# Kernel optimization log

Measured on AMD Instinct MI355X. Metric: run time of the kernel, lower is better.

## Reference

```python
import jax, jax.numpy as jnp
import numpy as np

# video grid and attention geometry (must match init_kwargs)
F_T, H_T, W_T = 4, 32, 32
K = 3                      # kernel_size (odd)
P = K // 2
T = F_T * H_T * W_T        # max_num_tokens = 4096
HEADS = 8
DIM_HEAD = 64
SCALE = DIM_HEAD ** -0.5
DIM = 512
INNER = HEADS * DIM_HEAD


def _build_window_indices():
    # flat token index grid, padded with sentinel T (out-of-range -> zero row after gather)
    idx = np.arange(T).reshape(F_T, H_T, W_T)
    padded = np.full((F_T + 2 * P, H_T + 2 * P, W_T + 2 * P), T, dtype=np.int64)
    padded[P:P + F_T, P:P + H_T, P:P + W_T] = idx
    # [T, K^3] neighborhood indices, kernel offsets in (kf, kh, kw) C-order (matches unfoldNd)
    win = np.lib.stride_tricks.sliding_window_view(padded, (K, K, K)).reshape(T, K ** 3)
    # causal: mask keys whose flat index is strictly in the future of the query
    causal = np.arange(T)[:, None] < win
    causal = np.concatenate([np.zeros((T, 1), dtype=bool), causal], axis=1)  # BOS column never masked
    return jnp.asarray(win), jnp.asarray(causal)

WIN_IDX, CAUSAL_MASK = _build_window_indices()


def setup_inputs() -> dict:
    key = jax.random.key(0)
    k0, k1, k2, k3 = jax.random.split(key, 4)
    n = T  # 1 BOS + (T-1) video tokens; padding logic pads body to exactly T tokens
    x = jax.random.normal(k0, (2, n, DIM), dtype=jnp.float32)
    Wq = jax.random.normal(k1, (DIM, INNER), dtype=jnp.float32) * (DIM ** -0.5)
    Wkv = jax.random.normal(k2, (DIM, 2 * INNER), dtype=jnp.float32) * (DIM ** -0.5)
    Wo = jax.random.normal(k3, (INNER, DIM), dtype=jnp.float32) * (INNER ** -0.5)
    bo = jnp.zeros((DIM,), dtype=jnp.float32)
    return {"x": x, "Wq": Wq, "Wkv": Wkv, "Wo": Wo, "bo": bo}


def _split_heads(t, b):
    # [b, n, h*d] -> [(b*h), n, d]
    n = t.shape[1]
    return t.reshape(b, n, HEADS, DIM_HEAD).transpose(0, 2, 1, 3).reshape(b * HEADS, n, DIM_HEAD)


def reference(x, Wq, Wkv, Wo, bo):
    b, n, _ = x.shape
    tpf = H_T * W_T
    padding = tpf - (n - 1) % tpf  # pads body tokens to a multiple of tokens_per_frame
    x = jnp.pad(x, ((0, 0), (0, padding), (0, 0)))
    q = x @ Wq
    k, v = jnp.split(x @ Wkv, 2, axis=-1)
    q, k, v = (_split_heads(t, b) for t in (q, k, v))
    bh = b * HEADS
    q = q[:, 1:] * SCALE            # drop BOS query; [bh, T, d]
    bos_v = v[:, :1]                # BOS attends only to itself -> its value passes through
    k_bos, k = k[:, :1], k[:, 1:]
    v_bos, v = v[:, :1], v[:, 1:]
    # gather K^3 3D neighborhoods; sentinel index T maps to a zero row
    zero_row = jnp.zeros((bh, 1, DIM_HEAD), dtype=k.dtype)
    k_nb = jnp.concatenate([k, zero_row], axis=1)[:, WIN_IDX]   # [bh, T, K^3, d]
    v_nb = jnp.concatenate([v, zero_row], axis=1)[:, WIN_IDX]
    # prepend global BOS key/value to every window
    k_nb = jnp.concatenate([jnp.broadcast_to(k_bos[:, :, None], (bh, T, 1, DIM_HEAD)), k_nb], axis=2)
    v_nb = jnp.concatenate([jnp.broadcast_to(v_bos[:, :, None], (bh, T, 1, DIM_HEAD)), v_nb], axis=2)
    sim = jnp.einsum('bid,bijd->bij', q, k_nb)                  # [bh, T, K^3+1]
    sim = jnp.where(CAUSAL_MASK[None], -jnp.finfo(sim.dtype).max, sim)
    attn = jax.nn.softmax(sim, axis=-1)
    out = jnp.einsum('bij,bijd->bid', attn, v_nb)               # [bh, T, d]
    out = jnp.concatenate([bos_v, out], axis=1)                 # [bh, T+1, d]
    np_tok = out.shape[1]
    out = out.reshape(b, HEADS, np_tok, DIM_HEAD).transpose(0, 2, 1, 3).reshape(b, np_tok, INNER)
    return (out @ Wo + bo)[:, :n]
```

## Files before the change

kernel.cpp:

```cpp
#include <hip/hip_runtime.h>


#define T_TOK   4096
#define DIM     512
#define NQKV    1536

typedef unsigned short u16;
typedef unsigned int   u32;
typedef unsigned long long u64;
typedef __attribute__((ext_vector_type(8))) short short8;
typedef __attribute__((ext_vector_type(4))) float f32x4;

__device__ __forceinline__ u16 f2bf(float f) {
    u32 u = __float_as_uint(f);
    return (u16)((u + 0x7fffu + ((u >> 16) & 1u)) >> 16);
}
__device__ __forceinline__ float b2f(u16 u) {
    return __uint_as_float(((u32)u) << 16);
}

__device__ __forceinline__ void gload_lds16(const void* g, void* l) {
    __builtin_amdgcn_global_load_lds(
        (const __attribute__((address_space(1))) void*)g,
        (__attribute__((address_space(3))) void*)l, 16, 0, 0);
}

__global__ void cast_all_kernel(const float4* __restrict__ x,
                                const float* __restrict__ Wq, const float* __restrict__ Wkv,
                                const float* __restrict__ Wo,
                                u16* __restrict__ xb, u16* __restrict__ Wt,
                                u16* __restrict__ Wot) {
    __shared__ float S[64 * 65];
    int blk = blockIdx.x;
    int tid = threadIdx.x;
    if (blk < 4096) {
        int i = blk * 256 + tid;
        float4 v = x[i];
        u64 pack = (u64)f2bf(v.x) | ((u64)f2bf(v.y) << 16) |
                   ((u64)f2bf(v.z) << 32) | ((u64)f2bf(v.w) << 48);
        ((u64*)xb)[i] = pack;
        return;
    }
    int isWo = blk >= 4288;
    int tIdx = isWo ? (blk - 4288) : (blk - 4096);
    int tn = tIdx >> 3, tk = tIdx & 7;
    #pragma unroll
    for (int p = 0; p < 16; ++p) {
        int kl = p * 4 + (tid >> 6), nl = tid & 63;
        int gk = tk * 64 + kl, gn = tn * 64 + nl;
        float v;
        if (isWo)            v = Wo[gk * 512 + gn];
        else if (gn < 512)   v = Wq[gk * 512 + gn];
        else                 v = Wkv[gk * 1024 + (gn - 512)];
        S[kl * 65 + nl] = v;
    }
    __syncthreads();
    u16* dst = isWo ? Wot : Wt;
    #pragma unroll
    for (int p = 0; p < 16; ++p) {
        int nl = p * 4 + (tid >> 6), kl = tid & 63;
        dst[(size_t)(tn * 64 + nl) * 512 + tk * 64 + kl] = f2bf(S[kl * 65 + nl]);
    }
}

template <int BM, int BN, int MODE>
__global__ __launch_bounds__(256)
void gemm_nt(const u16* __restrict__ A, const u16* __restrict__ B,
             void* __restrict__ Cv, const float* __restrict__ bias,
             int lda, int ldb, int ldc) {
    constexpr int K = 512, BK = 32, KSTEPS = K / BK;
    constexpr int ACH = BM * 4;
    constexpr int NCH = (BM + BN) * 4;
    constexpr int NLD = NCH / 256;
    constexpr int ABYTES = BM * 64;
    constexpr int HALF = (BM + BN) * 64;
    constexpr int MI = BM / 32, NJ = BN / 32;
    __shared__ __align__(16) char lds[2 * HALF];
    const int tid  = threadIdx.x;
    const int lane = tid & 63, wave = tid >> 6;
    const int quad = lane >> 4, mrow = lane & 15;
    const int wm = wave >> 1, wn = wave & 1;
    const int bm = blockIdx.y, bn = blockIdx.x;

    const char* gptr[NLD];
    char*       lptr[NLD];
    #pragma unroll
    for (int it = 0; it < NLD; ++it) {
        int c   = it * 256 + tid;
        int inB = (c >= ACH);
        int a   = inB ? c - ACH : c;
        int r   = a >> 2;
        int kc  = ((a & 3) - (r >> 1)) & 3;
        int row = (inB ? bn * BN : bm * BM) + r;
        const u16* base = inB ? B : A;
        int ld = inB ? ldb : lda;
        gptr[it] = (const char*)(base + (size_t)row * ld + kc * 8);
        lptr[it] = (char*)lds + (it * 256 + wave * 64) * 16;
    }
    const char* aLds[MI];
    const char* bLds[NJ];
    #pragma unroll
    for (int i = 0; i < MI; ++i) {
        int ra = wm * (BM / 2) + i * 16 + mrow;
        aLds[i] = lds + (ra * 4 + ((quad + (ra >> 1)) & 3)) * 16;
    }
    #pragma unroll
    for (int j = 0; j < NJ; ++j) {
        int rb = wn * (BN / 2) + j * 16 + mrow;
        bLds[j] = lds + ABYTES + (rb * 4 + ((quad + (rb >> 1)) & 3)) * 16;
    }

    f32x4 acc[MI][NJ] = {};
    #pragma unroll
    for (int it = 0; it < NLD; ++it)
        gload_lds16(gptr[it], lptr[it]);

    #pragma unroll
    for (int ks = 0; ks < KSTEPS; ++ks) {
        const int cur = ks & 1;
        if (ks + 1 < KSTEPS) {
            #pragma unroll
            for (int it = 0; it < NLD; ++it)
                gload_lds16(gptr[it] + 2 * (ks + 1) * BK, lptr[it] + (cur ^ 1) * HALF);
            asm volatile("s_waitcnt vmcnt(%0)" :: "i"(NLD) : "memory");
        } else {
            asm volatile("s_waitcnt vmcnt(0)" ::: "memory");
        }
        asm volatile("s_barrier" ::: "memory");

        short8 af[MI], bf[NJ];
        #pragma unroll
        for (int i = 0; i < MI; ++i) af[i] = *(const short8*)(aLds[i] + cur * HALF);
        #pragma unroll
        for (int j = 0; j < NJ; ++j) bf[j] = *(const short8*)(bLds[j] + cur * HALF);
        #pragma unroll
        for (int i = 0; i < MI; ++i)
            #pragma unroll
            for (int j = 0; j < NJ; ++j)
                acc[i][j] = __builtin_amdgcn_mfma_f32_16x16x32_bf16(af[i], bf[j], acc[i][j], 0, 0, 0);
        asm volatile("s_waitcnt lgkmcnt(0)" ::: "memory");
        asm volatile("s_barrier" ::: "memory");
    }

    #pragma unroll
    for (int i = 0; i < MI; ++i) {
        #pragma unroll
        for (int j = 0; j < NJ; ++j) {
            int colg = bn * BN + wn * (BN / 2) + j * 16 + mrow;
            #pragma unroll
            for (int r = 0; r < 4; ++r) {
                int rowg = bm * BM + wm * (BM / 2) + i * 16 + quad * 4 + r;
                if (MODE == 0) {
                    ((u16*)Cv)[(size_t)rowg * ldc + colg] = f2bf(acc[i][j][r]);
                } else {
                    ((float*)Cv)[(size_t)rowg * ldc + colg] = acc[i][j][r] + bias[colg];
                }
            }
        }
    }
}

__global__ __launch_bounds__(256)
void attn_kernel(const u16* __restrict__ QKV, u16* __restrict__ O) {
    const int wid  = blockIdx.x * 4 + (threadIdx.x >> 6);
    const int lane = threadIdx.x & 63;
    const int bh = wid >> 12;
    const int ti = wid & 4095;
    const int b = bh >> 3, h = bh & 7;
    const size_t baseQ = (size_t)b * T_TOK * NQKV;
    const size_t baseO = (size_t)b * T_TOK * DIM;

    if (ti == 0) {
        O[baseO + h * 64 + lane] = QKV[baseQ + 1024 + h * 64 + lane];
        return;
    }
    const int t = ti - 1;
    const int f = t >> 10, hh = (t >> 5) & 31, ww = t & 31;

    const int j = lane >> 2, g = lane & 3;
    int jm1 = j - 1;
    int dh9 = ((jm1 * 11) >> 5) - 1;
    int dw9 = jm1 - (dh9 + 1) * 3 - 1;
    int df = (j >= 1 && j <= 9) ? -1 : 0;
    int dh = (j >= 1 && j <= 9) ? dh9 : ((j >= 10 && j <= 12) ? -1 : 0);
    int dw = (j >= 1 && j <= 9) ? dw9 :
             ((j >= 10 && j <= 12) ? (j - 11) : ((j == 13) ? -1 : 0));
    int nf = f + df, nh = hh + dh, nw = ww + dw;
    int valid = (nf >= 0) && ((unsigned)nh < 32u) && ((unsigned)nw < 32u)
                && (j >= 1) && (j <= 14);
    int p = valid ? (t + 1 + df * 1024 + dh * 32 + dw) : 0;
    int score_on = valid || (j == 0);

    const u16* qrow = QKV + baseQ + (size_t)(t + 1) * NQKV + h * 64 + g * 16;
    short8 q0 = *(const short8*)qrow;
    short8 q1 = *(const short8*)(qrow + 8);
    const u16* krow = QKV + baseQ + (size_t)p * NQKV + 512 + h * 64 + g * 16;
    short8 k0 = *(const short8*)krow;
    short8 k1 = *(const short8*)(krow + 8);
    float s = 0.f;
    #pragma unroll
    for (int i = 0; i < 8; ++i) {
        s = fmaf(b2f((u16)q0[i]), b2f((u16)k0[i]), s);
        s = fmaf(b2f((u16)q1[i]), b2f((u16)k1[i]), s);
    }
    s += __shfl_xor(s, 1);
    s += __shfl_xor(s, 2);
    s *= 0.125f;
    s = score_on ? s : -3.0e38f;

    float m = s;
    #pragma unroll
    for (int off = 4; off <= 32; off <<= 1) m = fmaxf(m, __shfl_xor(m, off));
    float pe = __expf(s - m);
    float l = pe;
    #pragma unroll
    for (int off = 4; off <= 32; off <<= 1) l += __shfl_xor(l, off);
    float pen = pe * __frcp_rn(l);
    u32 voff = (u32)p * 3072u;

    float acc = 0.f;
    const char* vb = (const char*)(QKV + baseQ + 1024 + h * 64 + lane);
    #pragma unroll
    for (int jj = 0; jj < 15; ++jj) {
        u32 o = (u32)__builtin_amdgcn_readlane((int)voff, jj * 4);
        float pj = __uint_as_float(
                     (u32)__builtin_amdgcn_readlane((int)__float_as_uint(pen), jj * 4));
        float vv = b2f(*(const u16*)(vb + o));
        acc = fmaf(pj, vv, acc);
    }
    O[baseO + (size_t)ti * DIM + h * 64 + lane] = f2bf(acc);
}

extern "C" void kernel_launch(void* const* d_in, const int* in_sizes, int n_in,
                              void* d_out, int out_size, void* d_ws, size_t ws_size,
                              hipStream_t stream) {
    const float* x   = (const float*)d_in[0];
    const float* Wq  = (const float*)d_in[1];
    const float* Wkv = (const float*)d_in[2];
    const float* Wo  = (const float*)d_in[3];
    const float* bo  = (const float*)d_in[4];
    float* out = (float*)d_out;
    char* ws = (char*)d_ws;

    u16* xb  = (u16*)(ws + 0);
    u16* Wt  = (u16*)(ws + 8388608);
    u16* Wot = (u16*)(ws + 9961472);
    u16* QKV = (u16*)(ws + 10485760);
    u16* O   = (u16*)(ws + 0);

    cast_all_kernel<<<dim3(4352), dim3(256), 0, stream>>>(
        (const float4*)x, Wq, Wkv, Wo, xb, Wt, Wot);
    gemm_nt<128, 128, 0><<<dim3(12, 64), dim3(256), 0, stream>>>(
        xb, Wt, (void*)QKV, nullptr, 512, 512, 1536);
    attn_kernel<<<dim3(16384), dim3(256), 0, stream>>>(QKV, O);
    gemm_nt<128, 64, 1><<<dim3(8, 64), dim3(256), 0, stream>>>(
        O, Wot, (void*)out, bo, 512, 512, 512);
}
```

Baseline: 138.8 us.

## Stage K/V halo patches in shared memory for neighborhood attention

Replaces the one-wave-per-query attention kernel with one block per 8x8 spatial patch, frame and head. Each block loads a two-frame 10x10 K/V halo plus the BOS row into LDS once, then loops over its 64 queries reading keys and values from LDS. This removes the repeated global gathers of neighbour K/V rows across queries. In exchange there are far fewer blocks and more serial work per wave, and K rows use an XOR-style swizzle to avoid bank conflicts.

```diff
diff --git a/kernel.cpp b/kernel.cpp
--- a/kernel.cpp
+++ b/kernel.cpp
@@ -161,22 +161,45 @@
 }
 
 __global__ __launch_bounds__(256)
-void attn_kernel(const u16* __restrict__ QKV, u16* __restrict__ O) {
-    const int wid  = blockIdx.x * 4 + (threadIdx.x >> 6);
-    const int lane = threadIdx.x & 63;
-    const int bh = wid >> 12;
-    const int ti = wid & 4095;
-    const int b = bh >> 3, h = bh & 7;
+void attn_patch(const u16* __restrict__ QKV, u16* __restrict__ O) {
+    __shared__ u16 Ksh[201 * 64];
+    __shared__ u16 Vsh[201 * 64];
+    const int blk = blockIdx.x;
+    const int b = blk >> 9, rem = blk & 511;
+    const int f = rem >> 7, pid = (rem >> 3) & 15, h = rem & 7;
+    const int ph = (pid >> 2) * 8, pw = (pid & 3) * 8;
     const size_t baseQ = (size_t)b * T_TOK * NQKV;
     const size_t baseO = (size_t)b * T_TOK * DIM;
-
-    if (ti == 0) {
-        O[baseO + h * 64 + lane] = QKV[baseQ + 1024 + h * 64 + lane];
-        return;
-    }
-    const int t = ti - 1;
-    const int f = t >> 10, hh = (t >> 5) & 31, ww = t & 31;
-
+    const int tid = threadIdx.x;
+
+    for (int c = tid; c < 201 * 16; c += 256) {
+        int row = c >> 4, pp = c & 15;
+        int kv = pp >> 3, part = pp & 7;
+        int p = 0, val = 1;
+        if (row < 200) {
+            int plane = row / 100, rr = row % 100;
+            int hz = ph - 1 + rr / 10, wz = pw - 1 + rr % 10;
+            int fz = f - 1 + plane;
+            val = (fz >= 0) && ((unsigned)hz < 32u) && ((unsigned)wz < 32u);
+            p = ((fz << 10) + (hz << 5) + wz) + 1;
+        }
+        int dpart = kv ? part : ((part + 2 * row) & 7);
+        u16* dst = (kv ? Vsh : Ksh) + row * 64 + dpart * 8;
+        if (val) {
+            const u16* src = QKV + baseQ + (size_t)p * NQKV +
+                             (kv ? 1024 : 512) + h * 64 + part * 8;
+            *(short8*)dst = *(const short8*)src;
+        } else {
+            short8 z = {};
+            *(short8*)dst = z;
+        }
+    }
+    __syncthreads();
+
+    if (f == 0 && pid == 0 && tid < 64)
+        O[baseO + h * 64 + tid] = Vsh[200 * 64 + tid];
+
+    const int wave = tid >> 6, lane = tid & 63;
     const int j = lane >> 2, g = lane & 3;
     int jm1 = j - 1;
     int dh9 = ((jm1 * 11) >> 5) - 1;
@@ -185,50 +208,58 @@
     int dh = (j >= 1 && j <= 9) ? dh9 : ((j >= 10 && j <= 12) ? -1 : 0);
     int dw = (j >= 1 && j <= 9) ? dw9 :
              ((j >= 10 && j <= 12) ? (j - 11) : ((j == 13) ? -1 : 0));
-    int nf = f + df, nh = hh + dh, nw = ww + dw;
-    int valid = (nf >= 0) && ((unsigned)nh < 32u) && ((unsigned)nw < 32u)
-                && (j >= 1) && (j <= 14);
-    int p = valid ? (t + 1 + df * 1024 + dh * 32 + dw) : 0;
-    int score_on = valid || (j == 0);
-
-    const u16* qrow = QKV + baseQ + (size_t)(t + 1) * NQKV + h * 64 + g * 16;
-    short8 q0 = *(const short8*)qrow;
-    short8 q1 = *(const short8*)(qrow + 8);
-    const u16* krow = QKV + baseQ + (size_t)p * NQKV + 512 + h * 64 + g * 16;
-    short8 k0 = *(const short8*)krow;
-    short8 k1 = *(const short8*)(krow + 8);
-    float s = 0.f;
-    #pragma unroll
-    for (int i = 0; i < 8; ++i) {
-        s = fmaf(b2f((u16)q0[i]), b2f((u16)k0[i]), s);
-        s = fmaf(b2f((u16)q1[i]), b2f((u16)k1[i]), s);
-    }
-    s += __shfl_xor(s, 1);
-    s += __shfl_xor(s, 2);
-    s *= 0.125f;
-    s = score_on ? s : -3.0e38f;
-
-    float m = s;
-    #pragma unroll
-    for (int off = 4; off <= 32; off <<= 1) m = fmaxf(m, __shfl_xor(m, off));
-    float pe = __expf(s - m);
-    float l = pe;
-    #pragma unroll
-    for (int off = 4; off <= 32; off <<= 1) l += __shfl_xor(l, off);
-    float pen = pe * __frcp_rn(l);
-    u32 voff = (u32)p * 3072u;
-
-    float acc = 0.f;
-    const char* vb = (const char*)(QKV + baseQ + 1024 + h * 64 + lane);
-    #pragma unroll
-    for (int jj = 0; jj < 15; ++jj) {
-        u32 o = (u32)__builtin_amdgcn_readlane((int)voff, jj * 4);
-        float pj = __uint_as_float(
-                     (u32)__builtin_amdgcn_readlane((int)__float_as_uint(pen), jj * 4));
-        float vv = b2f(*(const u16*)(vb + o));
-        acc = fmaf(pj, vv, acc);
-    }
-    O[baseO + (size_t)ti * DIM + h * 64 + lane] = f2bf(acc);
+    const int jok = (j >= 1) && (j <= 14) && (f + df >= 0);
+
+    for (int s = 0; s < 16; ++s) {
+        int qi = wave * 16 + s;
+        int hq = ph + (qi >> 3), wq = pw + (qi & 7);
+        int t = (f << 10) + (hq << 5) + wq;
+        if (t == 4095) continue;
+        int nh = hq + dh, nw = wq + dw;
+        int valid = jok && ((unsigned)nh < 32u) && ((unsigned)nw < 32u);
+        int r = (j == 0) ? 200
+              : (valid ? ((df + 1) * 100 + (dh + hq - ph + 1) * 10 +
+                          (dw + wq - pw + 1)) : 200);
+        int score_on = valid || (j == 0);
+
+        const u16* qrow = QKV + baseQ + (size_t)(t + 1) * NQKV + h * 64 + g * 16;
+        short8 q0 = *(const short8*)qrow;
+        short8 q1 = *(const short8*)(qrow + 8);
+        int c0 = (2 * g + 2 * r) & 7;
+        const u16* kp = Ksh + r * 64 + c0 * 8;
+        short8 k0 = *(const short8*)kp;
+        short8 k1 = *(const short8*)(kp + 8);
+
+        float sdot = 0.f;
+        #pragma unroll
+        for (int i = 0; i < 8; ++i) {
+            sdot = fmaf(b2f((u16)q0[i]), b2f((u16)k0[i]), sdot);
+            sdot = fmaf(b2f((u16)q1[i]), b2f((u16)k1[i]), sdot);
+        }
+        sdot += __shfl_xor(sdot, 1);
+        sdot += __shfl_xor(sdot, 2);
+        sdot *= 0.125f;
+        sdot = score_on ? sdot : -3.0e38f;
+
+        float m = sdot;
+        #pragma unroll
+        for (int off = 4; off <= 32; off <<= 1) m = fmaxf(m, __shfl_xor(m, off));
+        float pe = __expf(sdot - m);
+        float l = pe;
+        #pragma unroll
+        for (int off = 4; off <= 32; off <<= 1) l += __shfl_xor(l, off);
+        float pen = pe * __frcp_rn(l);
+
+        float acc = 0.f;
+        #pragma unroll
+        for (int jj = 0; jj < 15; ++jj) {
+            int   rr2 = __builtin_amdgcn_readlane(r, jj * 4);
+            float pj  = __uint_as_float(
+                          (u32)__builtin_amdgcn_readlane((int)__float_as_uint(pen), jj * 4));
+            acc = fmaf(pj, b2f(Vsh[rr2 * 64 + lane]), acc);
+        }
+        O[baseO + (size_t)(t + 1) * DIM + h * 64 + lane] = f2bf(acc);
+    }
 }
 
 extern "C" void kernel_launch(void* const* d_in, const int* in_sizes, int n_in,
@@ -252,7 +283,7 @@
         (const float4*)x, Wq, Wkv, Wo, xb, Wt, Wot);
     gemm_nt<128, 128, 0><<<dim3(12, 64), dim3(256), 0, stream>>>(
         xb, Wt, (void*)QKV, nullptr, 512, 512, 1536);
-    attn_kernel<<<dim3(16384), dim3(256), 0, stream>>>(QKV, O);
+    attn_patch<<<dim3(1024), dim3(256), 0, stream>>>(QKV, O);
     gemm_nt<128, 64, 1><<<dim3(8, 64), dim3(256), 0, stream>>>(
         O, Wot, (void*)out, bo, 512, 512, 512);
 }
```

Measured after the change: 156.5 us. 1.13x slower.
